# Performance work log

Measured on AMD Instinct MI355X. Metric: run time of the kernel, lower is better.

## Reference

```python
import jax, jax.numpy as jnp
import numpy as np

HIDDEN = 1024
NUM_HEADS = 16
HEAD_DIM = HIDDEN // NUM_HEADS


def setup_inputs() -> dict:
    key = jax.random.key(0)
    ks = jax.random.split(key, 9)
    s = 0.02
    return {
        "x": jax.random.normal(ks[0], (2, 2048, HIDDEN), dtype=jnp.float32),
        "wq": jax.random.normal(ks[1], (HIDDEN, HIDDEN), dtype=jnp.float32) * s,
        "bq": jnp.zeros((HIDDEN,), dtype=jnp.float32),
        "wk": jax.random.normal(ks[2], (HIDDEN, HIDDEN), dtype=jnp.float32) * s,
        "bk": jnp.zeros((HIDDEN,), dtype=jnp.float32),
        "wv": jax.random.normal(ks[3], (HIDDEN, HIDDEN), dtype=jnp.float32) * s,
        "bv": jnp.zeros((HIDDEN,), dtype=jnp.float32),
        "wo": jax.random.normal(ks[4], (HIDDEN, HIDDEN), dtype=jnp.float32) * s,
        "bo": jnp.zeros((HIDDEN,), dtype=jnp.float32),
    }


def reference(x, wq, bq, wk, bk, wv, bv, wo, bo):
    B, S, H = x.shape
    # torch nn.Linear: y = x @ W.T + b
    q = x @ wq.T + bq
    k = x @ wk.T + bk
    v = x @ wv.T + bv
    # [B, S, nH, dH] -> [B, nH, S, dH]
    q = q.reshape(B, S, NUM_HEADS, HEAD_DIM).transpose(0, 2, 1, 3)
    k = k.reshape(B, S, NUM_HEADS, HEAD_DIM).transpose(0, 2, 1, 3)
    v = v.reshape(B, S, NUM_HEADS, HEAD_DIM).transpose(0, 2, 1, 3)
    scores = jnp.einsum("bhqd,bhkd->bhqk", q, k)
    probs = jax.nn.softmax(scores / jnp.sqrt(jnp.float32(HEAD_DIM)), axis=-1)
    context = jnp.einsum("bhqk,bhkd->bhqd", probs, v)
    context = context.transpose(0, 2, 1, 3).reshape(B, S, H)
    return context @ wo.T + bo
```

## Files before the change

### kernel.cpp

```cpp
#include <hip/hip_runtime.h>
#include <hip/hip_bf16.h>
#include <math.h>

#define HID   1024
#define NHEAD 16
#define DHEAD 64
#define BATCH 2
#define SEQ   2048
#define TOK   (BATCH*SEQ)

typedef float f32x4  __attribute__((ext_vector_type(4)));
typedef short short8 __attribute__((ext_vector_type(8)));

__device__ __forceinline__ unsigned short f2bf(float f) {
    unsigned int u = __float_as_uint(f);
    u += 0x7FFFu + ((u >> 16) & 1u);
    return (unsigned short)(u >> 16);
}

__device__ __forceinline__ unsigned pk2(float lo, float hi) {
    union { __hip_bfloat162 h; unsigned u; } cv;
    cv.h = __float22bfloat162_rn(make_float2(lo, hi));
    return cv.u;
}

__device__ __forceinline__ void gll16(const unsigned short* g, unsigned short* l) {
    __builtin_amdgcn_global_load_lds(
        (const __attribute__((address_space(1))) void*)g,
        (__attribute__((address_space(3))) void*)l, 16, 0, 0);
}

__global__ __launch_bounds__(256) void cvt_bf16(const float* __restrict__ in,
                                                unsigned short* __restrict__ out, int n8) {
    int i = blockIdx.x * 256 + threadIdx.x;
    if (i >= n8) return;
    const float4* p = (const float4*)in;
    float4 a = p[2*i], b = p[2*i+1];
    uint4 r;
    r.x = pk2(a.x, a.y); r.y = pk2(a.z, a.w);
    r.z = pk2(b.x, b.y); r.w = pk2(b.z, b.w);
    ((uint4*)out)[i] = r;
}

__global__ __launch_bounds__(256) void cvt_bf16_w4(
    const float* __restrict__ i0, const float* __restrict__ i1,
    const float* __restrict__ i2, const float* __restrict__ i3,
    unsigned short* __restrict__ o0, unsigned short* __restrict__ o1,
    unsigned short* __restrict__ o2, unsigned short* __restrict__ o3, int n8) {
    int i = blockIdx.x * 256 + threadIdx.x;
    if (i >= n8) return;
    int z = blockIdx.y;
    const float* in = (z==0)?i0:((z==1)?i1:((z==2)?i2:i3));
    unsigned short* out = (z==0)?o0:((z==1)?o1:((z==2)?o2:o3));
    const float4* p = (const float4*)in;
    float4 a = p[2*i], b = p[2*i+1];
    uint4 r;
    r.x = pk2(a.x, a.y); r.y = pk2(a.z, a.w);
    r.z = pk2(b.x, b.y); r.w = pk2(b.z, b.w);
    ((uint4*)out)[i] = r;
}

template<int NZ, bool OUTF32>
__global__ __launch_bounds__(256, 3) void gemm_gll(
    const unsigned short* __restrict__ A,
    const unsigned short* __restrict__ W0, const unsigned short* __restrict__ W1,
    const unsigned short* __restrict__ W2,
    const float* __restrict__ b0, const float* __restrict__ b1, const float* __restrict__ b2,
    void* __restrict__ C0, void* __restrict__ C1, void* __restrict__ C2,
    int M, int N, int K)
{
    __shared__ unsigned short As[128*32];
    __shared__ unsigned short Ws[128*32];

    const unsigned short* W = W0; const float* bias = b0; void* C = C0;
    int z = 0;
    if (NZ > 1) {
        z = blockIdx.z;
        W    = (z==0) ? W0 : ((z==1) ? W1 : W2);
        bias = (z==0) ? b0 : ((z==1) ? b1 : b2);
        C    = (z==0) ? C0 : ((z==1) ? C1 : C2);
    }
    const int tid  = threadIdx.x;
    const int l15  = tid & 15, quad = (tid >> 4) & 3, w = tid >> 6;
    const int wm   = (w >> 1) * 64, wn = (w & 1) * 64;
    const int m0   = blockIdx.y * 128, n0 = blockIdx.x * 128;

    const int lane = tid & 63, w4 = tid >> 6;
    const int grow = lane >> 2;
    const int gchk = (lane & 3) ^ (grow & 3);
    const unsigned short* pa0 = A + (size_t)(m0      + w4*16 + grow) * K + gchk*8;
    const unsigned short* pa1 = A + (size_t)(m0 + 64 + w4*16 + grow) * K + gchk*8;
    const unsigned short* pw0 = W + (size_t)(n0      + w4*16 + grow) * K + gchk*8;
    const unsigned short* pw1 = W + (size_t)(n0 + 64 + w4*16 + grow) * K + gchk*8;
    unsigned short* lA0 = &As[(w4*16)      * 32];
    unsigned short* lA1 = &As[(64 + w4*16) * 32];
    unsigned short* lW0 = &Ws[(w4*16)      * 32];
    unsigned short* lW1 = &Ws[(64 + w4*16) * 32];

    const int rchk = ((l15 & 3) );

    f32x4 acc[4][4] = {};

    for (int k0 = 0; k0 < K; k0 += 32) {
        gll16(pa0, lA0); gll16(pa1, lA1);
        gll16(pw0, lW0); gll16(pw1, lW1);
        pa0 += 32; pa1 += 32; pw0 += 32; pw1 += 32;
        __syncthreads();

        short8 af[4], bfv[4];
        const int co = (quad ^ rchk) * 8;
        #pragma unroll
        for (int mi = 0; mi < 4; ++mi) af[mi]  = *(const short8*)&As[(wm + mi*16 + l15)*32 + co];
        #pragma unroll
        for (int ni = 0; ni < 4; ++ni) bfv[ni] = *(const short8*)&Ws[(wn + ni*16 + l15)*32 + co];
        #pragma unroll
        for (int mi = 0; mi < 4; ++mi)
            #pragma unroll
            for (int ni = 0; ni < 4; ++ni)
                acc[mi][ni] = __builtin_amdgcn_mfma_f32_16x16x32_bf16(af[mi], bfv[ni], acc[mi][ni], 0, 0, 0);
        __syncthreads();
    }

    float bv[4];
    #pragma unroll
    for (int ni = 0; ni < 4; ++ni) bv[ni] = bias[n0 + wn + ni*16 + l15];

    if (NZ == 3 && z == 2) {
        #pragma unroll
        for (int mi = 0; mi < 4; ++mi)
            #pragma unroll
            for (int ni = 0; ni < 4; ++ni) {
                const int row0 = m0 + wm + mi*16 + quad*4;
                const int col  = n0 + wn + ni*16 + l15;
                const int hh = col >> 6, dd = col & 63;
                const int bb = row0 >> 11, ss = row0 & 2047;
                ushort4 r4;
                r4.x = f2bf(acc[mi][ni][0] + bv[ni]);
                r4.y = f2bf(acc[mi][ni][1] + bv[ni]);
                r4.z = f2bf(acc[mi][ni][2] + bv[ni]);
                r4.w = f2bf(acc[mi][ni][3] + bv[ni]);
                *(ushort4*)((unsigned short*)C + ((size_t)(bb*NHEAD + hh)*DHEAD + dd)*SEQ + ss) = r4;
            }
    } else {
        #pragma unroll
        for (int mi = 0; mi < 4; ++mi)
            #pragma unroll
            for (int ni = 0; ni < 4; ++ni)
                #pragma unroll
                for (int r = 0; r < 4; ++r) {
                    const int row = m0 + wm + mi*16 + quad*4 + r;
                    const int col = n0 + wn + ni*16 + l15;
                    const float val = acc[mi][ni][r] + bv[ni];
                    if (OUTF32) ((float*)C)[(size_t)row*N + col] = val;
                    else ((unsigned short*)C)[(size_t)row*N + col] = f2bf(val);
                }
    }
}

__global__ __launch_bounds__(256, 1) void attn_v3(
    const unsigned short* __restrict__ Qg, const unsigned short* __restrict__ Kg,
    const unsigned short* __restrict__ vT, unsigned short* __restrict__ Og)
{
    __shared__ unsigned short Ks[2][64][64];
    __shared__ unsigned short VT[2][64][64];
    __shared__ unsigned short Pw[4][64][64];
    unsigned short* Qs = &Pw[0][0][0];

    const int tid  = threadIdx.x;
    const int l15  = tid & 15, quad = (tid >> 4) & 3, w = tid >> 6;
    const int b    = blockIdx.z, h = blockIdx.y;
    const int q0   = blockIdx.x * 256;
    const size_t rowbase = (size_t)b * SEQ;
    const int    cbase   = h * DHEAD;
    const size_t vbase   = (size_t)(b*NHEAD + h) * DHEAD * SEQ;

    {
        const unsigned short* src = Qg + (rowbase + q0 + tid) * HID + cbase;
        #pragma unroll
        for (int j = 0; j < 8; ++j)
            *(uint4*)&Qs[tid*64 + ((j ^ (tid & 7)) * 8)] = *(const uint4*)(src + j*8);
    }
    short8 qa[4][2];
    #pragma unroll
    for (int mi = 0; mi < 4; ++mi)
        #pragma unroll
        for (int s2 = 0; s2 < 2; ++s2)
            qa[mi][s2] = *(const short8*)&Qs[(w*64 + mi*16 + l15)*64 + (((s2*4 + quad) ^ (l15 & 7)) * 8)];

    const int sr = tid >> 2, sc = (tid & 3) * 16;
    const int c0 = (sc >> 3) ^ (sr & 7);
    const int c1 = ((sc >> 3) + 1) ^ (sr & 7);
    {
        const unsigned short* ks = Kg + (rowbase + sr) * HID + cbase + sc;
        const unsigned short* vs = vT + vbase + (size_t)sr * SEQ + sc;
        *(uint4*)&Ks[0][sr][c0*8] = *(const uint4*)ks;
        *(uint4*)&Ks[0][sr][c1*8] = *(const uint4*)(ks + 8);
        *(uint4*)&VT[0][sr][c0*8] = *(const uint4*)vs;
        *(uint4*)&VT[0][sr][c1*8] = *(const uint4*)(vs + 8);
    }

    f32x4 o[4][4] = {};
    f32x4 lsum[4] = {};
    const int fco = ((quad) ^ (l15 & 7));

    for (int kt = 0; kt < SEQ/64; ++kt) {
        const int buf = kt & 1;
        __syncthreads();

        uint4 kr0, kr1, vr0, vr1;
        const bool pre = (kt + 1 < SEQ/64);
        if (pre) {
            const unsigned short* ks = Kg + (rowbase + (kt+1)*64 + sr) * HID + cbase + sc;
            const unsigned short* vs = vT + vbase + (size_t)sr * SEQ + (kt+1)*64 + sc;
            kr0 = *(const uint4*)ks; kr1 = *(const uint4*)(ks + 8);
            vr0 = *(const uint4*)vs; vr1 = *(const uint4*)(vs + 8);
        }

        f32x4 s[4][4] = {};
        #pragma unroll
        for (int s2 = 0; s2 < 2; ++s2) {
            short8 kf[4];
            #pragma unroll
            for (int nt = 0; nt < 4; ++nt)
                kf[nt] = *(const short8*)&Ks[buf][nt*16 + l15][((s2*4 + quad) ^ (l15 & 7)) * 8];
            #pragma unroll
            for (int mi = 0; mi < 4; ++mi)
                #pragma unroll
                for (int nt = 0; nt < 4; ++nt)
                    s[mi][nt] = __builtin_amdgcn_mfma_f32_16x16x32_bf16(qa[mi][s2], kf[nt], s[mi][nt], 0, 0, 0);
        }

        const int odd = l15 & 1;
        #pragma unroll
        for (int mi = 0; mi < 4; ++mi) {
            #pragma unroll
            for (int nt = 0; nt < 4; ++nt) {
                const float p0 = __expf(s[mi][nt][0] * 0.125f);
                const float p1 = __expf(s[mi][nt][1] * 0.125f);
                const float p2 = __expf(s[mi][nt][2] * 0.125f);
                const float p3 = __expf(s[mi][nt][3] * 0.125f);
                lsum[mi][0] += p0; lsum[mi][1] += p1;
                lsum[mi][2] += p2; lsum[mi][3] += p3;
                const float x0 = __shfl_xor(p0, 1);
                const float x1 = __shfl_xor(p1, 1);
                const float x2 = __shfl_xor(p2, 1);
                const float x3 = __shfl_xor(p3, 1);
                const unsigned da = odd ? pk2(x2, p2) : pk2(p0, x0);
                const unsigned db = odd ? pk2(x3, p3) : pk2(p1, x1);
                const int rb = mi*16 + quad*4 + odd*2;
                const int cp = nt*16 + (l15 & ~1);
                const int ch = cp >> 3;
                const int in = (cp & 7);
                *(unsigned*)&Pw[w][rb  ][((ch ^ ( rb      & 7)) * 8) + in] = da;
                *(unsigned*)&Pw[w][rb+1][((ch ^ ((rb + 1) & 7)) * 8) + in] = db;
            }
        }

        #pragma unroll
        for (int s2 = 0; s2 < 2; ++s2) {
            short8 pa[4], vf[4];
            #pragma unroll
            for (int mi = 0; mi < 4; ++mi)
                pa[mi] = *(const short8*)&Pw[w][mi*16 + l15][((s2*4 + quad) ^ (l15 & 7)) * 8];
            #pragma unroll
            for (int nt = 0; nt < 4; ++nt)
                vf[nt] = *(const short8*)&VT[buf][nt*16 + l15][((s2*4 + quad) ^ (l15 & 7)) * 8];
            #pragma unroll
            for (int mi = 0; mi < 4; ++mi)
                #pragma unroll
                for (int nt = 0; nt < 4; ++nt)
                    o[mi][nt] = __builtin_amdgcn_mfma_f32_16x16x32_bf16(pa[mi], vf[nt], o[mi][nt], 0, 0, 0);
        }

        if (pre) {
            const int nb = buf ^ 1;
            *(uint4*)&Ks[nb][sr][c0*8] = kr0;
            *(uint4*)&Ks[nb][sr][c1*8] = kr1;
            *(uint4*)&VT[nb][sr][c0*8] = vr0;
            *(uint4*)&VT[nb][sr][c1*8] = vr1;
        }
    }

    float linv[4][4];
    #pragma unroll
    for (int mi = 0; mi < 4; ++mi)
        #pragma unroll
        for (int r = 0; r < 4; ++r) {
            float l = lsum[mi][r];
            l += __shfl_xor(l, 1, 16);
            l += __shfl_xor(l, 2, 16);
            l += __shfl_xor(l, 4, 16);
            l += __shfl_xor(l, 8, 16);
            linv[mi][r] = 1.0f / l;
        }
    #pragma unroll
    for (int mi = 0; mi < 4; ++mi)
        #pragma unroll
        for (int nt = 0; nt < 4; ++nt)
            #pragma unroll
            for (int r = 0; r < 4; ++r) {
                const size_t row = rowbase + q0 + w*64 + mi*16 + quad*4 + r;
                Og[row * HID + cbase + nt*16 + l15] = f2bf(o[mi][nt][r] * linv[mi][r]);
            }
}

extern "C" void kernel_launch(void* const* d_in, const int* in_sizes, int n_in,
                              void* d_out, int out_size, void* d_ws, size_t ws_size,
                              hipStream_t stream)
{
    const float* x  = (const float*)d_in[0];
    const float* wq = (const float*)d_in[1];
    const float* bq = (const float*)d_in[2];
    const float* wk = (const float*)d_in[3];
    const float* bk = (const float*)d_in[4];
    const float* wv = (const float*)d_in[5];
    const float* bv = (const float*)d_in[6];
    const float* wo = (const float*)d_in[7];
    const float* bo = (const float*)d_in[8];
    float* out = (float*)d_out;

    unsigned short* xb  = (unsigned short*)d_ws;
    unsigned short* wqb = xb  + (size_t)TOK * HID;
    unsigned short* wkb = wqb + (size_t)HID * HID;
    unsigned short* wvb = wkb + (size_t)HID * HID;
    unsigned short* wob = wvb + (size_t)HID * HID;
    unsigned short* qb  = wob + (size_t)HID * HID;
    unsigned short* kb  = qb  + (size_t)TOK * HID;
    unsigned short* vtb = kb  + (size_t)TOK * HID;
    unsigned short* cb  = vtb + (size_t)TOK * HID;

    const dim3 blk(256);
    cvt_bf16<<<dim3(TOK*HID/8/256), blk, 0, stream>>>(x, xb, TOK*HID/8);
    cvt_bf16_w4<<<dim3(HID*HID/8/256, 4), blk, 0, stream>>>(
        wq, wk, wv, wo, wqb, wkb, wvb, wob, HID*HID/8);

    gemm_gll<3, false><<<dim3(HID/128, TOK/128, 3), blk, 0, stream>>>(
        xb, wqb, wkb, wvb, bq, bk, bv, qb, kb, vtb, TOK, HID, HID);

    attn_v3<<<dim3(SEQ/256, NHEAD, BATCH), blk, 0, stream>>>(qb, kb, vtb, cb);

    gemm_gll<1, true><<<dim3(HID/128, TOK/128, 1), blk, 0, stream>>>(
        cb, wob, wob, wob, bo, bo, bo, out, out, out, TOK, HID, HID);
}
```

Measured before the change: 233.7 us.

## Split attention keys across two blocks and add partial-context reduce kernel

The attention kernel now splits the key sequence into two halves handled by separate blocks, doubling the grid, and allows two blocks per CU. Each block writes unnormalized bf16 partial outputs and row sums, and a new reduce kernel adds them and normalizes before the output projection. The MFMA operand order is also transposed so probabilities are written per query row without cross-lane shuffles. This trades extra global traffic and a kernel launch for better CU occupancy, at some precision risk from bf16 partials.

Result: faster. 210.0 us (-10.1%).

```diff
diff --git a/kernel.cpp b/kernel.cpp
--- a/kernel.cpp
+++ b/kernel.cpp
@@ -97,7 +97,7 @@
     unsigned short* lW0 = &Ws[(w4*16)      * 32];
     unsigned short* lW1 = &Ws[(64 + w4*16) * 32];
 
-    const int rchk = ((l15 & 3) );
+    const int rchk = (l15 & 3);
 
     f32x4 acc[4][4] = {};
 
@@ -157,42 +157,46 @@
     }
 }
 
-__global__ __launch_bounds__(256, 1) void attn_v3(
+__global__ __launch_bounds__(256, 2) void attn_v4(
     const unsigned short* __restrict__ Qg, const unsigned short* __restrict__ Kg,
-    const unsigned short* __restrict__ vT, unsigned short* __restrict__ Og)
+    const unsigned short* __restrict__ vT,
+    unsigned short* __restrict__ pO0, unsigned short* __restrict__ pO1,
+    float* __restrict__ pl)
 {
     __shared__ unsigned short Ks[2][64][64];
     __shared__ unsigned short VT[2][64][64];
-    __shared__ unsigned short Pw[4][64][64];
-    unsigned short* Qs = &Pw[0][0][0];
+    __shared__ unsigned short PTs[4*64*64];
 
     const int tid  = threadIdx.x;
     const int l15  = tid & 15, quad = (tid >> 4) & 3, w = tid >> 6;
-    const int b    = blockIdx.z, h = blockIdx.y;
+    const int z    = blockIdx.z;
+    const int b    = z & 1, half = z >> 1;
+    const int h    = blockIdx.y;
     const int q0   = blockIdx.x * 256;
     const size_t rowbase = (size_t)b * SEQ;
     const int    cbase   = h * DHEAD;
     const size_t vbase   = (size_t)(b*NHEAD + h) * DHEAD * SEQ;
+    const int    keybase = half * (SEQ/2);
 
     {
         const unsigned short* src = Qg + (rowbase + q0 + tid) * HID + cbase;
         #pragma unroll
         for (int j = 0; j < 8; ++j)
-            *(uint4*)&Qs[tid*64 + ((j ^ (tid & 7)) * 8)] = *(const uint4*)(src + j*8);
+            *(uint4*)&PTs[tid*64 + ((j ^ (tid & 7)) * 8)] = *(const uint4*)(src + j*8);
     }
     short8 qa[4][2];
     #pragma unroll
-    for (int mi = 0; mi < 4; ++mi)
+    for (int nq = 0; nq < 4; ++nq)
         #pragma unroll
         for (int s2 = 0; s2 < 2; ++s2)
-            qa[mi][s2] = *(const short8*)&Qs[(w*64 + mi*16 + l15)*64 + (((s2*4 + quad) ^ (l15 & 7)) * 8)];
+            qa[nq][s2] = *(const short8*)&PTs[(w*64 + nq*16 + l15)*64 + (((s2*4 + quad) ^ (l15 & 7)) * 8)];
 
     const int sr = tid >> 2, sc = (tid & 3) * 16;
     const int c0 = (sc >> 3) ^ (sr & 7);
     const int c1 = ((sc >> 3) + 1) ^ (sr & 7);
     {
-        const unsigned short* ks = Kg + (rowbase + sr) * HID + cbase + sc;
-        const unsigned short* vs = vT + vbase + (size_t)sr * SEQ + sc;
+        const unsigned short* ks = Kg + (rowbase + keybase + sr) * HID + cbase + sc;
+        const unsigned short* vs = vT + vbase + (size_t)sr * SEQ + keybase + sc;
         *(uint4*)&Ks[0][sr][c0*8] = *(const uint4*)ks;
         *(uint4*)&Ks[0][sr][c1*8] = *(const uint4*)(ks + 8);
         *(uint4*)&VT[0][sr][c0*8] = *(const uint4*)vs;
@@ -200,18 +204,18 @@
     }
 
     f32x4 o[4][4] = {};
-    f32x4 lsum[4] = {};
-    const int fco = ((quad) ^ (l15 & 7));
-
-    for (int kt = 0; kt < SEQ/64; ++kt) {
+    float lsum[4] = {0.f, 0.f, 0.f, 0.f};
+    unsigned short* myPT = &PTs[w*64*64];
+
+    for (int kt = 0; kt < SEQ/2/64; ++kt) {
         const int buf = kt & 1;
         __syncthreads();
 
         uint4 kr0, kr1, vr0, vr1;
-        const bool pre = (kt + 1 < SEQ/64);
+        const bool pre = (kt + 1 < SEQ/2/64);
         if (pre) {
-            const unsigned short* ks = Kg + (rowbase + (kt+1)*64 + sr) * HID + cbase + sc;
-            const unsigned short* vs = vT + vbase + (size_t)sr * SEQ + (kt+1)*64 + sc;
+            const unsigned short* ks = Kg + (rowbase + keybase + (kt+1)*64 + sr) * HID + cbase + sc;
+            const unsigned short* vs = vT + vbase + (size_t)sr * SEQ + keybase + (kt+1)*64 + sc;
             kr0 = *(const uint4*)ks; kr1 = *(const uint4*)(ks + 8);
             vr0 = *(const uint4*)vs; vr1 = *(const uint4*)(vs + 8);
         }
@@ -219,57 +223,45 @@
         f32x4 s[4][4] = {};
         #pragma unroll
         for (int s2 = 0; s2 < 2; ++s2) {
-            short8 kf[4];
-            #pragma unroll
-            for (int nt = 0; nt < 4; ++nt)
-                kf[nt] = *(const short8*)&Ks[buf][nt*16 + l15][((s2*4 + quad) ^ (l15 & 7)) * 8];
+            short8 kfr[4];
+            #pragma unroll
+            for (int mi = 0; mi < 4; ++mi)
+                kfr[mi] = *(const short8*)&Ks[buf][mi*16 + l15][((s2*4 + quad) ^ (l15 & 7)) * 8];
             #pragma unroll
             for (int mi = 0; mi < 4; ++mi)
                 #pragma unroll
-                for (int nt = 0; nt < 4; ++nt)
-                    s[mi][nt] = __builtin_amdgcn_mfma_f32_16x16x32_bf16(qa[mi][s2], kf[nt], s[mi][nt], 0, 0, 0);
-        }
-
-        const int odd = l15 & 1;
-        #pragma unroll
-        for (int mi = 0; mi < 4; ++mi) {
-            #pragma unroll
-            for (int nt = 0; nt < 4; ++nt) {
-                const float p0 = __expf(s[mi][nt][0] * 0.125f);
-                const float p1 = __expf(s[mi][nt][1] * 0.125f);
-                const float p2 = __expf(s[mi][nt][2] * 0.125f);
-                const float p3 = __expf(s[mi][nt][3] * 0.125f);
-                lsum[mi][0] += p0; lsum[mi][1] += p1;
-                lsum[mi][2] += p2; lsum[mi][3] += p3;
-                const float x0 = __shfl_xor(p0, 1);
-                const float x1 = __shfl_xor(p1, 1);
-                const float x2 = __shfl_xor(p2, 1);
-                const float x3 = __shfl_xor(p3, 1);
-                const unsigned da = odd ? pk2(x2, p2) : pk2(p0, x0);
-                const unsigned db = odd ? pk2(x3, p3) : pk2(p1, x1);
-                const int rb = mi*16 + quad*4 + odd*2;
-                const int cp = nt*16 + (l15 & ~1);
-                const int ch = cp >> 3;
-                const int in = (cp & 7);
-                *(unsigned*)&Pw[w][rb  ][((ch ^ ( rb      & 7)) * 8) + in] = da;
-                *(unsigned*)&Pw[w][rb+1][((ch ^ ((rb + 1) & 7)) * 8) + in] = db;
+                for (int nq = 0; nq < 4; ++nq)
+                    s[mi][nq] = __builtin_amdgcn_mfma_f32_16x16x32_bf16(kfr[mi], qa[nq][s2], s[mi][nq], 0, 0, 0);
+        }
+
+        #pragma unroll
+        for (int mi = 0; mi < 4; ++mi)
+            #pragma unroll
+            for (int nq = 0; nq < 4; ++nq) {
+                const float p0 = __expf(s[mi][nq][0] * 0.125f);
+                const float p1 = __expf(s[mi][nq][1] * 0.125f);
+                const float p2 = __expf(s[mi][nq][2] * 0.125f);
+                const float p3 = __expf(s[mi][nq][3] * 0.125f);
+                lsum[nq] += (p0 + p1) + (p2 + p3);
+                uint2 u; u.x = pk2(p0, p1); u.y = pk2(p2, p3);
+                const int off = (((2*mi + (quad >> 1)) ^ (l15 & 7)) * 8) + (quad & 1) * 4;
+                *(uint2*)&myPT[(nq*16 + l15)*64 + off] = u;
             }
-        }
-
-        #pragma unroll
-        for (int s2 = 0; s2 < 2; ++s2) {
-            short8 pa[4], vf[4];
-            #pragma unroll
-            for (int mi = 0; mi < 4; ++mi)
-                pa[mi] = *(const short8*)&Pw[w][mi*16 + l15][((s2*4 + quad) ^ (l15 & 7)) * 8];
-            #pragma unroll
-            for (int nt = 0; nt < 4; ++nt)
-                vf[nt] = *(const short8*)&VT[buf][nt*16 + l15][((s2*4 + quad) ^ (l15 & 7)) * 8];
-            #pragma unroll
-            for (int mi = 0; mi < 4; ++mi)
+
+        #pragma unroll
+        for (int ks2 = 0; ks2 < 2; ++ks2) {
+            short8 ptb[4], vfr[4];
+            #pragma unroll
+            for (int nq = 0; nq < 4; ++nq)
+                ptb[nq] = *(const short8*)&myPT[(nq*16 + l15)*64 + ((ks2*4 + quad) ^ (l15 & 7)) * 8];
+            #pragma unroll
+            for (int md = 0; md < 4; ++md)
+                vfr[md] = *(const short8*)&VT[buf][md*16 + l15][((ks2*4 + quad) ^ (l15 & 7)) * 8];
+            #pragma unroll
+            for (int md = 0; md < 4; ++md)
                 #pragma unroll
-                for (int nt = 0; nt < 4; ++nt)
-                    o[mi][nt] = __builtin_amdgcn_mfma_f32_16x16x32_bf16(pa[mi], vf[nt], o[mi][nt], 0, 0, 0);
+                for (int nq = 0; nq < 4; ++nq)
+                    o[md][nq] = __builtin_amdgcn_mfma_f32_16x16x32_bf16(vfr[md], ptb[nq], o[md][nq], 0, 0, 0);
         }
 
         if (pre) {
@@ -281,27 +273,51 @@
         }
     }
 
-    float linv[4][4];
+    unsigned short* pO = half ? pO1 : pO0;
     #pragma unroll
-    for (int mi = 0; mi < 4; ++mi)
-        #pragma unroll
-        for (int r = 0; r < 4; ++r) {
-            float l = lsum[mi][r];
-            l += __shfl_xor(l, 1, 16);
-            l += __shfl_xor(l, 2, 16);
-            l += __shfl_xor(l, 4, 16);
-            l += __shfl_xor(l, 8, 16);
-            linv[mi][r] = 1.0f / l;
-        }
-    #pragma unroll
-    for (int mi = 0; mi < 4; ++mi)
-        #pragma unroll
-        for (int nt = 0; nt < 4; ++nt)
-            #pragma unroll
-            for (int r = 0; r < 4; ++r) {
-                const size_t row = rowbase + q0 + w*64 + mi*16 + quad*4 + r;
-                Og[row * HID + cbase + nt*16 + l15] = f2bf(o[mi][nt][r] * linv[mi][r]);
-            }
+    for (int nq = 0; nq < 4; ++nq) {
+        float l = lsum[nq];
+        l += __shfl_xor(l, 16);
+        l += __shfl_xor(l, 32);
+        if (quad == 0)
+            pl[(((size_t)half * BATCH + b) * NHEAD + h) * SEQ + q0 + w*64 + nq*16 + l15] = l;
+        const size_t row = rowbase + q0 + w*64 + nq*16 + l15;
+        #pragma unroll
+        for (int md = 0; md < 4; ++md) {
+            ushort4 u;
+            u.x = f2bf(o[md][nq][0]); u.y = f2bf(o[md][nq][1]);
+            u.z = f2bf(o[md][nq][2]); u.w = f2bf(o[md][nq][3]);
+            *(ushort4*)&pO[row * HID + cbase + md*16 + quad*4] = u;
+        }
+    }
+}
+
+__device__ __forceinline__ unsigned addpair(unsigned a, unsigned c, float inv) {
+    float a0 = __uint_as_float(a << 16), a1 = __uint_as_float(a & 0xffff0000u);
+    float c0 = __uint_as_float(c << 16), c1 = __uint_as_float(c & 0xffff0000u);
+    return pk2((a0 + c0) * inv, (a1 + c1) * inv);
+}
+
+__global__ __launch_bounds__(256) void reduce_ctx(
+    const unsigned short* __restrict__ p0, const unsigned short* __restrict__ p1,
+    const float* __restrict__ pl, unsigned short* __restrict__ ctx)
+{
+    const int i  = blockIdx.x * 256 + threadIdx.x;
+    const int e0 = i * 8;
+    const int t  = e0 >> 10;
+    const int h  = (e0 & 1023) >> 6;
+    const int b  = t >> 11, q = t & 2047;
+    const float l0 = pl[(((size_t)0 * BATCH + b) * NHEAD + h) * SEQ + q];
+    const float l1 = pl[(((size_t)1 * BATCH + b) * NHEAD + h) * SEQ + q];
+    const float inv = 1.f / (l0 + l1);
+    uint4 a = ((const uint4*)p0)[i];
+    uint4 c = ((const uint4*)p1)[i];
+    uint4 r;
+    r.x = addpair(a.x, c.x, inv);
+    r.y = addpair(a.y, c.y, inv);
+    r.z = addpair(a.z, c.z, inv);
+    r.w = addpair(a.w, c.w, inv);
+    ((uint4*)ctx)[i] = r;
 }
 
 extern "C" void kernel_launch(void* const* d_in, const int* in_sizes, int n_in,
@@ -337,8 +353,11 @@
     gemm_gll<3, false><<<dim3(HID/128, TOK/128, 3), blk, 0, stream>>>(
         xb, wqb, wkb, wvb, bq, bk, bv, qb, kb, vtb, TOK, HID, HID);
 
-    attn_v3<<<dim3(SEQ/256, NHEAD, BATCH), blk, 0, stream>>>(qb, kb, vtb, cb);
+    attn_v4<<<dim3(SEQ/256, NHEAD, 4), blk, 0, stream>>>(
+        qb, kb, vtb, cb, xb, (float*)wqb);
+
+    reduce_ctx<<<dim3(TOK*HID/8/256), blk, 0, stream>>>(cb, xb, (float*)wqb, qb);
 
     gemm_gll<1, true><<<dim3(HID/128, TOK/128, 1), blk, 0, stream>>>(
-        cb, wob, wob, wob, bo, bo, bo, out, out, out, TOK, HID, HID);
-}
+        qb, wob, wob, wob, bo, bo, bo, out, out, out, TOK, HID, HID);
+}
```
